# Kernel optimization log

Hardware: AMD Instinct MI355X
Metric: run time of the kernel (lower is better)

Reference implementation:

```python
import jax, jax.numpy as jnp
import numpy as np

DIM = 1024
N_HEADS = 16
HEAD_DIM = 64
SEQ = 2048
BATCH = 2


def setup_inputs() -> dict:
    key = jax.random.key(0)
    ks = jax.random.split(key, 7)
    scale = 1.0 / np.sqrt(DIM)
    return {
        "q": jax.random.normal(ks[0], (BATCH, SEQ, DIM), dtype=jnp.float32),
        "k": jax.random.normal(ks[1], (BATCH, SEQ, DIM), dtype=jnp.float32),
        "v": jax.random.normal(ks[2], (BATCH, SEQ, DIM), dtype=jnp.float32),
        "wq": jax.random.normal(ks[3], (DIM, DIM), dtype=jnp.float32) * scale,
        "wk": jax.random.normal(ks[4], (DIM, DIM), dtype=jnp.float32) * scale,
        "wv": jax.random.normal(ks[5], (DIM, DIM), dtype=jnp.float32) * scale,
        "wo": jax.random.normal(ks[6], (DIM, DIM), dtype=jnp.float32) * scale,
    }


def reference(q, k, v, wq, wk, wv, wo):
    B, S, D = q.shape
    # Linear layers: y = x @ W.T (torch nn.Linear convention)
    qh = (q @ wq.T).reshape(B, S, N_HEADS, HEAD_DIM).transpose(0, 2, 1, 3)  # [B,H,S,hd]
    kh = (k @ wk.T).reshape(B, S, N_HEADS, HEAD_DIM).transpose(0, 2, 1, 3)
    vh = (v @ wv.T).reshape(B, S, N_HEADS, HEAD_DIM).transpose(0, 2, 1, 3)
    score = jnp.einsum('bhqd,bhkd->bhqk', qh, kh) / jnp.sqrt(jnp.float32(HEAD_DIM))
    # causal mask: upper triangle (j > i) set to -inf
    causal = jnp.tril(jnp.ones((S, S), dtype=bool))
    score = jnp.where(causal[None, None], score, -jnp.inf)
    attn = jax.nn.softmax(score, axis=-1)
    out = jnp.einsum('bhqk,bhkd->bhqd', attn, vh)  # [B,H,S,hd]
    out = out.transpose(0, 2, 1, 3).reshape(B, S, D)
    return out @ wo.T
```

## Files before the change

### kernel.cpp

```cpp
#include <hip/hip_runtime.h>

typedef unsigned short u16;
typedef unsigned int   u32;
typedef __bf16 bf16x8 __attribute__((ext_vector_type(8)));
typedef float  f32x4  __attribute__((ext_vector_type(4)));
typedef unsigned short u16x4 __attribute__((ext_vector_type(4)));
typedef unsigned short u16x8 __attribute__((ext_vector_type(8)));
typedef unsigned int   u32x2 __attribute__((ext_vector_type(2)));
typedef unsigned int   u32x4 __attribute__((ext_vector_type(4)));

#define DIM   1024
#define SEQ   2048
#define NH    16
#define HD    64
#define NBATCH 2

#define NEG_INF (-__builtin_inff())
#define QSCALE 0.1803368801111204f


__device__ __forceinline__ u16 f2bf(float f) {
  unsigned u = __float_as_uint(f);
  unsigned r = (u + 0x7FFFu + ((u >> 16) & 1u)) >> 16;
  return (u16)r;
}

__device__ __forceinline__ u32 pkbf(float a, float b) {
#if __has_builtin(__builtin_amdgcn_cvt_pk_bf16_f32)
  typedef __bf16 bf16x2 __attribute__((ext_vector_type(2)));
  bf16x2 t = __builtin_amdgcn_cvt_pk_bf16_f32(a, b);
  return __builtin_bit_cast(u32, t);
#else
  return (u32)f2bf(a) | ((u32)f2bf(b) << 16);
#endif
}

__device__ __forceinline__ void gload16(const void* g, void* lds_uniform) {
  __builtin_amdgcn_global_load_lds(
      (__attribute__((address_space(1))) void*)(size_t)g,
      (__attribute__((address_space(3))) void*)lds_uniform,
      16, 0, 0);
}


__global__ __launch_bounds__(256) void cvt_all(
    const float* __restrict__ q, const float* __restrict__ k, const float* __restrict__ v,
    const float* __restrict__ wq, const float* __restrict__ wk, const float* __restrict__ wv,
    const float* __restrict__ wo, u16* __restrict__ ws) {
  const size_t M = 1u << 20;
  int b = blockIdx.x;
  const float* src;
  u16* dst;
  int idx;
  if (b < 6144) {
    int t = b >> 11; idx = b & 2047;
    src = (t == 0) ? q : (t == 1) ? k : v;
    dst = ws + (size_t)t * 4 * M;
  } else {
    int t = (b - 6144) >> 9; idx = (b - 6144) & 511;
    src = (t == 0) ? wq : (t == 1) ? wk : (t == 2) ? wv : wo;
    dst = ws + (12 + (size_t)t) * M;
  }
  size_t i = ((size_t)idx * 256 + threadIdx.x) * 8;
  float4 a = *(const float4*)(src + i);
  float4 c = *(const float4*)(src + i + 4);
  u16x8 o;
  o[0] = f2bf(a.x); o[1] = f2bf(a.y); o[2] = f2bf(a.z); o[3] = f2bf(a.w);
  o[4] = f2bf(c.x); o[5] = f2bf(c.y); o[6] = f2bf(c.z); o[7] = f2bf(c.w);
  *(u16x8*)(dst + i) = o;
}


__device__ __forceinline__ void gemm128_core(const u16* __restrict__ A,
                                             const u16* __restrict__ W,
                                             int bm, int bn,
                                             u16* lds, f32x4 (&acc)[4][4]) {
  const int K = 1024;
  const int tid = threadIdx.x;
  const int wave = tid >> 6, lane = tid & 63;
  const int quad = lane >> 4, l15 = lane & 15;
  const int warp_m = wave >> 1, warp_n = wave & 1;

  const int c0 = wave * 128 + lane, c1 = c0 + 64;
  const u16* Ag0 = A + (size_t)(bm * 128 + (c0 >> 2)) * K + (c0 & 3) * 8;
  const u16* Ag1 = A + (size_t)(bm * 128 + (c1 >> 2)) * K + (c1 & 3) * 8;
  const u16* Wg0 = W + (size_t)(bn * 128 + (c0 >> 2)) * K + (c0 & 3) * 8;
  const u16* Wg1 = W + (size_t)(bn * 128 + (c1 >> 2)) * K + (c1 & 3) * 8;
  const int lA0 = (wave * 2 + 0) * 512;
  const int lA1 = (wave * 2 + 1) * 512;
  const int lB0 = 4096 + (wave * 2 + 0) * 512;
  const int lB1 = 4096 + (wave * 2 + 1) * 512;

  gload16(Ag0, lds + lA0);
  gload16(Ag1, lds + lA1);
  gload16(Wg0, lds + lB0);
  gload16(Wg1, lds + lB1);

  for (int k0 = 0; k0 < K; k0 += 32) {
    const int buf = (k0 >> 5) & 1;
    u16* cur = lds + buf * 8192;
    __syncthreads();
    if (k0 + 32 < K) {
      u16* nxt = lds + (buf ^ 1) * 8192;
      gload16(Ag0 + k0 + 32, nxt + lA0);
      gload16(Ag1 + k0 + 32, nxt + lA1);
      gload16(Wg0 + k0 + 32, nxt + lB0);
      gload16(Wg1 + k0 + 32, nxt + lB1);
    }

    bf16x8 af[4], bfr[4];
#pragma unroll
    for (int i = 0; i < 4; ++i) {
      af[i]  = *(const bf16x8*)(cur + (warp_m * 64 + i * 16 + l15) * 32 + quad * 8);
      bfr[i] = *(const bf16x8*)(cur + 4096 + (warp_n * 64 + i * 16 + l15) * 32 + quad * 8);
    }
#pragma unroll
    for (int i = 0; i < 4; ++i)
#pragma unroll
      for (int j = 0; j < 4; ++j)
        acc[i][j] = __builtin_amdgcn_mfma_f32_16x16x32_bf16(af[i], bfr[j], acc[i][j], 0, 0, 0);
  }
}

__global__ __launch_bounds__(256) void gemm_qkv(
    const u16* __restrict__ qb, const u16* __restrict__ kb, const u16* __restrict__ vb,
    const u16* __restrict__ wq, const u16* __restrict__ wk, const u16* __restrict__ wv,
    u16* __restrict__ Qo, u16* __restrict__ Ko, u16* __restrict__ Vt) {
  __shared__ __align__(16) u16 lds[2][8192];
  const int id = blockIdx.x;
  const int c = id & 7, bn = (id >> 3) & 7, t = id >> 6;
  const int g = c + 8 * t;
  const int bm = g & 31, z = g >> 5;

  const u16* A = (z == 0) ? qb : (z == 1) ? kb : vb;
  const u16* W = (z == 0) ? wq : (z == 1) ? wk : wv;
  f32x4 acc[4][4] = {};
  gemm128_core(A, W, bm, bn, &lds[0][0], acc);

  const int tid = threadIdx.x;
  const int wave = tid >> 6, lane = tid & 63;
  const int quad = lane >> 4, l15 = lane & 15;
  const int warp_m = wave >> 1, warp_n = wave & 1;
#pragma unroll
  for (int i = 0; i < 4; ++i)
#pragma unroll
    for (int j = 0; j < 4; ++j) {
      int s0 = bm * 128 + warp_m * 64 + i * 16 + quad * 4;
      int n  = bn * 128 + warp_n * 64 + j * 16 + l15;
      int bb = s0 >> 11, sl0 = s0 & 2047, h = n >> 6, d = n & 63;
      if (z == 2) {
        int pos = (sl0 & ~63) | (sl0 & 32) | ((sl0 & 12) << 1) | ((sl0 & 16) >> 2);
        int psw = (pos & ~63) | ((((pos >> 3) & 7) ^ (d & 7)) << 3) | (pos & 7);
        u16x4 pv;
        pv[0] = f2bf(acc[i][j][0]); pv[1] = f2bf(acc[i][j][1]);
        pv[2] = f2bf(acc[i][j][2]); pv[3] = f2bf(acc[i][j][3]);
        *(u16x4*)(Vt + ((size_t)(bb * NH + h) * HD + d) * SEQ + psw) = pv;
      } else if (z == 1) {
#pragma unroll
        for (int r = 0; r < 4; ++r) {
          int s = sl0 + r;
          int dsw = (((d >> 3) ^ (s & 7)) << 3) | (d & 7);
          Ko[((size_t)(bb * NH + h) * SEQ + s) * HD + dsw] = f2bf(acc[i][j][r]);
        }
      } else {
#pragma unroll
        for (int r = 0; r < 4; ++r)
          Qo[((size_t)(bb * NH + h) * SEQ + sl0 + r) * HD + d] = f2bf(acc[i][j][r] * QSCALE);
      }
    }
}

__global__ __launch_bounds__(256) void gemm_out(
    const u16* __restrict__ A, const u16* __restrict__ W, float* __restrict__ Out) {
  __shared__ __align__(16) u16 lds[2][8192];
  const int id = blockIdx.x;
  const int bn = (id >> 3) & 7;
  const int bm = (id & 7) + 8 * (id >> 6);
  f32x4 acc[4][4] = {};
  gemm128_core(A, W, bm, bn, &lds[0][0], acc);

  const int tid = threadIdx.x;
  const int wave = tid >> 6, lane = tid & 63;
  const int quad = lane >> 4, l15 = lane & 15;
  const int warp_m = wave >> 1, warp_n = wave & 1;
#pragma unroll
  for (int i = 0; i < 4; ++i)
#pragma unroll
    for (int j = 0; j < 4; ++j)
#pragma unroll
      for (int r = 0; r < 4; ++r) {
        int m = bm * 128 + warp_m * 64 + i * 16 + quad * 4 + r;
        int n = bn * 128 + warp_n * 64 + j * 16 + l15;
        Out[(size_t)m * DIM + n] = acc[i][j][r];
      }
}


__global__ __launch_bounds__(256) void attn_kernel(
    const u16* __restrict__ Q, const u16* __restrict__ K,
    const u16* __restrict__ Vt, u16* __restrict__ O) {
  __shared__ __align__(16) u16 Kl[2][4096];
  __shared__ __align__(16) u16 Vl[2][4096];

  const int tid = threadIdx.x;
  const int wave = tid >> 6, lane = tid & 63;
  const int quad = lane >> 4, l15 = lane & 15;
  const int bx = blockIdx.x;
  const int bh = bx & 31;
  const int qt = 31 - (bx >> 5);
  const int b = bh >> 4, h = bh & 15;

  const u16* qbase = Q + ((size_t)bh * SEQ + qt * 64 + wave * 16 + l15) * HD + quad * 8;
  const bf16x8 qf0 = *(const bf16x8*)(qbase);
  const bf16x8 qf1 = *(const bf16x8*)(qbase + 32);

  bf16x8 ones;
#pragma unroll
  for (int i = 0; i < 8; ++i) ones[i] = (__bf16)1.0f;

  f32x4 o[4] = {};
  f32x4 o4 = {};
  float m_run = NEG_INF;

  const int c0 = wave * 128 + lane, c1 = c0 + 64;
  const u16* Ksrc = K + (size_t)bh * SEQ * HD;
  const u16* Vsrc = Vt + (size_t)bh * HD * SEQ;
  const int sw0 = ((quad ^ (l15 & 7)) << 3);
  const int sw1 = (((4 + quad) ^ (l15 & 7)) << 3);

  {
    gload16(Ksrc + (size_t)c0 * 8, &Kl[0][(wave * 2 + 0) * 512]);
    gload16(Ksrc + (size_t)c1 * 8, &Kl[0][(wave * 2 + 1) * 512]);
    gload16(Vsrc + (size_t)(c0 >> 3) * SEQ + (c0 & 7) * 8, &Vl[0][(wave * 2 + 0) * 512]);
    gload16(Vsrc + (size_t)(c1 >> 3) * SEQ + (c1 & 7) * 8, &Vl[0][(wave * 2 + 1) * 512]);
  }

  for (int kt = 0; kt <= qt; ++kt) {
    const int buf = kt & 1;
    __syncthreads();
    if (kt < qt) {
      const int nb = buf ^ 1;
      const size_t kb = (size_t)(kt + 1) * 64;
      gload16(Ksrc + (kb * HD) + (size_t)c0 * 8, &Kl[nb][(wave * 2 + 0) * 512]);
      gload16(Ksrc + (kb * HD) + (size_t)c1 * 8, &Kl[nb][(wave * 2 + 1) * 512]);
      gload16(Vsrc + (size_t)(c0 >> 3) * SEQ + kb + (c0 & 7) * 8, &Vl[nb][(wave * 2 + 0) * 512]);
      gload16(Vsrc + (size_t)(c1 >> 3) * SEQ + kb + (c1 & 7) * 8, &Vl[nb][(wave * 2 + 1) * 512]);
    }

    f32x4 s[4];
#pragma unroll
    for (int kn = 0; kn < 4; ++kn) {
      const u16* arow = &Kl[buf][(kn * 16 + l15) * 64];
      bf16x8 kf0 = *(const bf16x8*)(arow + sw0);
      bf16x8 kf1 = *(const bf16x8*)(arow + sw1);
      f32x4 z = {};
      z = __builtin_amdgcn_mfma_f32_16x16x32_bf16(kf0, qf0, z, 0, 0, 0);
      z = __builtin_amdgcn_mfma_f32_16x16x32_bf16(kf1, qf1, z, 0, 0, 0);
      s[kn] = z;
    }

    if (kt == qt) {
      const int qloc = wave * 16 + l15;
#pragma unroll
      for (int kn = 0; kn < 4; ++kn)
#pragma unroll
        for (int r = 0; r < 4; ++r)
          if (kn * 16 + quad * 4 + r > qloc) s[kn][r] = NEG_INF;
    }

    float mr = NEG_INF;
#pragma unroll
    for (int kn = 0; kn < 4; ++kn)
#pragma unroll
      for (int r = 0; r < 4; ++r) mr = fmaxf(mr, s[kn][r]);
    mr = fmaxf(mr, __shfl_xor(mr, 16));
    mr = fmaxf(mr, __shfl_xor(mr, 32));
    const float mnew = fmaxf(m_run, mr);
    const float alpha = __builtin_amdgcn_exp2f(m_run - mnew);
    m_run = mnew;
#pragma unroll
    for (int kn = 0; kn < 4; ++kn)
#pragma unroll
      for (int r = 0; r < 4; ++r)
        s[kn][r] = __builtin_amdgcn_exp2f(s[kn][r] - mnew);

    u32x4 t0, t1;
    t0[0] = pkbf(s[0][0], s[0][1]); t0[1] = pkbf(s[0][2], s[0][3]);
    t0[2] = pkbf(s[1][0], s[1][1]); t0[3] = pkbf(s[1][2], s[1][3]);
    t1[0] = pkbf(s[2][0], s[2][1]); t1[1] = pkbf(s[2][2], s[2][3]);
    t1[2] = pkbf(s[3][0], s[3][1]); t1[3] = pkbf(s[3][2], s[3][3]);
    bf16x8 pf0 = __builtin_bit_cast(bf16x8, t0);
    bf16x8 pf1 = __builtin_bit_cast(bf16x8, t1);

#pragma unroll
    for (int n = 0; n < 4; ++n)
#pragma unroll
      for (int r = 0; r < 4; ++r) o[n][r] *= alpha;
#pragma unroll
    for (int r = 0; r < 4; ++r) o4[r] *= alpha;

    o4 = __builtin_amdgcn_mfma_f32_16x16x32_bf16(ones, pf0, o4, 0, 0, 0);
    o4 = __builtin_amdgcn_mfma_f32_16x16x32_bf16(ones, pf1, o4, 0, 0, 0);

#pragma unroll
    for (int n = 0; n < 4; ++n) {
      const u16* vrow = &Vl[buf][(n * 16 + l15) * 64];
      bf16x8 vf0 = *(const bf16x8*)(vrow + sw0);
      bf16x8 vf1 = *(const bf16x8*)(vrow + sw1);
      o[n] = __builtin_amdgcn_mfma_f32_16x16x32_bf16(vf0, pf0, o[n], 0, 0, 0);
      o[n] = __builtin_amdgcn_mfma_f32_16x16x32_bf16(vf1, pf1, o[n], 0, 0, 0);
    }
  }

  const float inv = 1.f / o4[0];
  const int srow = qt * 64 + wave * 16 + l15;
  u16* obase = O + ((size_t)b * SEQ + srow) * DIM + h * HD + quad * 4;
#pragma unroll
  for (int n = 0; n < 4; ++n) {
    u32x2 st;
    st[0] = pkbf(o[n][0] * inv, o[n][1] * inv);
    st[1] = pkbf(o[n][2] * inv, o[n][3] * inv);
    *(u32x2*)(obase + n * 16) = st;
  }
}


extern "C" void kernel_launch(void* const* d_in, const int* in_sizes, int n_in,
                              void* d_out, int out_size, void* d_ws, size_t ws_size,
                              hipStream_t stream) {
  (void)in_sizes; (void)n_in; (void)out_size; (void)ws_size;
  const float* q  = (const float*)d_in[0];
  const float* k  = (const float*)d_in[1];
  const float* v  = (const float*)d_in[2];
  const float* wq = (const float*)d_in[3];
  const float* wk = (const float*)d_in[4];
  const float* wv = (const float*)d_in[5];
  const float* wo = (const float*)d_in[6];

  u16* ws = (u16*)d_ws;
  const size_t EL = 1u << 20;
  u16* QB = ws + 0 * EL;
  u16* KB = ws + 4 * EL;
  u16* VB = ws + 8 * EL;
  u16* WQ = ws + 12 * EL;
  u16* WK = ws + 13 * EL;
  u16* WV = ws + 14 * EL;
  u16* WO = ws + 15 * EL;
  u16* Qw = ws + 16 * EL;
  u16* Kw = ws + 20 * EL;
  u16* Vtw = ws + 24 * EL;
  u16* AO = ws + 28 * EL;

  cvt_all<<<8192, 256, 0, stream>>>(q, k, v, wq, wk, wv, wo, ws);
  gemm_qkv<<<768, 256, 0, stream>>>(QB, KB, VB, WQ, WK, WV, Qw, Kw, Vtw);
  attn_kernel<<<1024, 256, 0, stream>>>(Qw, Kw, Vtw, AO);
  gemm_out<<<256, 256, 0, stream>>>(AO, WO, (float*)d_out);
}
```

Baseline: 200.6 us.

## Fuse activation bf16 conversion into QKV GEMM, swizzle LDS, retile out-proj

The separate conversion pass over the fp32 q/k/v activations is removed. The QKV GEMM now loads fp32 rows into registers, packs them to bf16 and stores them into LDS with an XOR swizzle, which removes a 48MB-ish round trip through workspace. W and A LDS layouts are swizzled to reduce bank conflicts. The output projection uses 128x64 tiles with 512 blocks for better CU occupancy, and the attention q-tile order is snaked for load balance. The cost is that the QKV GEMM does its A-operand conversion and register staging inside the main loop.

Result: slower. 222.5 us (+10.9%).

```diff
diff --git a/kernel.cpp b/kernel.cpp
--- a/kernel.cpp
+++ b/kernel.cpp
@@ -43,24 +43,15 @@
 }
 
 
-__global__ __launch_bounds__(256) void cvt_all(
-    const float* __restrict__ q, const float* __restrict__ k, const float* __restrict__ v,
-    const float* __restrict__ wq, const float* __restrict__ wk, const float* __restrict__ wv,
-    const float* __restrict__ wo, u16* __restrict__ ws) {
+__global__ __launch_bounds__(256) void cvt_w(
+    const float* __restrict__ wq, const float* __restrict__ wk,
+    const float* __restrict__ wv, const float* __restrict__ wo,
+    u16* __restrict__ ws) {
   const size_t M = 1u << 20;
   int b = blockIdx.x;
-  const float* src;
-  u16* dst;
-  int idx;
-  if (b < 6144) {
-    int t = b >> 11; idx = b & 2047;
-    src = (t == 0) ? q : (t == 1) ? k : v;
-    dst = ws + (size_t)t * 4 * M;
-  } else {
-    int t = (b - 6144) >> 9; idx = (b - 6144) & 511;
-    src = (t == 0) ? wq : (t == 1) ? wk : (t == 2) ? wv : wo;
-    dst = ws + (12 + (size_t)t) * M;
-  }
+  int t = b >> 9, idx = b & 511;
+  const float* src = (t == 0) ? wq : (t == 1) ? wk : (t == 2) ? wv : wo;
+  u16* dst = ws + (size_t)t * M;
   size_t i = ((size_t)idx * 256 + threadIdx.x) * 8;
   float4 a = *(const float4*)(src + i);
   float4 c = *(const float4*)(src + i + 4);
@@ -71,10 +62,10 @@
 }
 
 
-__device__ __forceinline__ void gemm128_core(const u16* __restrict__ A,
-                                             const u16* __restrict__ W,
-                                             int bm, int bn,
-                                             u16* lds, f32x4 (&acc)[4][4]) {
+__device__ __forceinline__ void gemm128f_core(const float* __restrict__ A,
+                                              const u16* __restrict__ W,
+                                              int bm, int bn,
+                                              u16* lds, f32x4 (&acc)[4][4]) {
   const int K = 1024;
   const int tid = threadIdx.x;
   const int wave = tid >> 6, lane = tid & 63;
@@ -82,37 +73,55 @@
   const int warp_m = wave >> 1, warp_n = wave & 1;
 
   const int c0 = wave * 128 + lane, c1 = c0 + 64;
-  const u16* Ag0 = A + (size_t)(bm * 128 + (c0 >> 2)) * K + (c0 & 3) * 8;
-  const u16* Ag1 = A + (size_t)(bm * 128 + (c1 >> 2)) * K + (c1 & 3) * 8;
-  const u16* Wg0 = W + (size_t)(bn * 128 + (c0 >> 2)) * K + (c0 & 3) * 8;
-  const u16* Wg1 = W + (size_t)(bn * 128 + (c1 >> 2)) * K + (c1 & 3) * 8;
-  const int lA0 = (wave * 2 + 0) * 512;
-  const int lA1 = (wave * 2 + 1) * 512;
+  const u16* Wg0 = W + (size_t)(bn * 128 + (c0 >> 2)) * K + (((c0 & 3) ^ ((c0 >> 3) & 3)) * 8);
+  const u16* Wg1 = W + (size_t)(bn * 128 + (c1 >> 2)) * K + (((c1 & 3) ^ ((c1 >> 3) & 3)) * 8);
   const int lB0 = 4096 + (wave * 2 + 0) * 512;
   const int lB1 = 4096 + (wave * 2 + 1) * 512;
 
-  gload16(Ag0, lds + lA0);
-  gload16(Ag1, lds + lA1);
+  const float* Ag[4];
+  int adst[4];
+#pragma unroll
+  for (int j = 0; j < 4; ++j) {
+    int ca = wave * 256 + 64 * j + lane;
+    int row = ca >> 3, ch = ca & 7;
+    Ag[j] = A + (size_t)(bm * 128 + row) * K + ch * 4;
+    adst[j] = row * 32 + (((ch >> 1) ^ ((row >> 1) & 3)) << 3) + (ch & 1) * 4;
+  }
+
+  float4 r[4];
+#pragma unroll
+  for (int j = 0; j < 4; ++j) r[j] = *(const float4*)(Ag[j]);
   gload16(Wg0, lds + lB0);
   gload16(Wg1, lds + lB1);
 
   for (int k0 = 0; k0 < K; k0 += 32) {
     const int buf = (k0 >> 5) & 1;
     u16* cur = lds + buf * 8192;
+
+#pragma unroll
+    for (int j = 0; j < 4; ++j) {
+      u32x2 wv;
+      wv[0] = pkbf(r[j].x, r[j].y);
+      wv[1] = pkbf(r[j].z, r[j].w);
+      *(u32x2*)(cur + adst[j]) = wv;
+    }
     __syncthreads();
+
     if (k0 + 32 < K) {
       u16* nxt = lds + (buf ^ 1) * 8192;
-      gload16(Ag0 + k0 + 32, nxt + lA0);
-      gload16(Ag1 + k0 + 32, nxt + lA1);
       gload16(Wg0 + k0 + 32, nxt + lB0);
       gload16(Wg1 + k0 + 32, nxt + lB1);
+#pragma unroll
+      for (int j = 0; j < 4; ++j) r[j] = *(const float4*)(Ag[j] + k0 + 32);
     }
 
     bf16x8 af[4], bfr[4];
 #pragma unroll
     for (int i = 0; i < 4; ++i) {
-      af[i]  = *(const bf16x8*)(cur + (warp_m * 64 + i * 16 + l15) * 32 + quad * 8);
-      bfr[i] = *(const bf16x8*)(cur + 4096 + (warp_n * 64 + i * 16 + l15) * 32 + quad * 8);
+      int ra = warp_m * 64 + i * 16 + l15;
+      int rb = warp_n * 64 + i * 16 + l15;
+      af[i]  = *(const bf16x8*)(cur + ra * 32 + ((quad ^ ((ra >> 1) & 3)) << 3));
+      bfr[i] = *(const bf16x8*)(cur + 4096 + rb * 32 + ((quad ^ ((rb >> 1) & 3)) << 3));
     }
 #pragma unroll
     for (int i = 0; i < 4; ++i)
@@ -123,7 +132,7 @@
 }
 
 __global__ __launch_bounds__(256) void gemm_qkv(
-    const u16* __restrict__ qb, const u16* __restrict__ kb, const u16* __restrict__ vb,
+    const float* __restrict__ qb, const float* __restrict__ kb, const float* __restrict__ vb,
     const u16* __restrict__ wq, const u16* __restrict__ wk, const u16* __restrict__ wv,
     u16* __restrict__ Qo, u16* __restrict__ Ko, u16* __restrict__ Vt) {
   __shared__ __align__(16) u16 lds[2][8192];
@@ -132,10 +141,10 @@
   const int g = c + 8 * t;
   const int bm = g & 31, z = g >> 5;
 
-  const u16* A = (z == 0) ? qb : (z == 1) ? kb : vb;
+  const float* A = (z == 0) ? qb : (z == 1) ? kb : vb;
   const u16* W = (z == 0) ? wq : (z == 1) ? wk : wv;
   f32x4 acc[4][4] = {};
-  gemm128_core(A, W, bm, bn, &lds[0][0], acc);
+  gemm128f_core(A, W, bm, bn, &lds[0][0], acc);
 
   const int tid = threadIdx.x;
   const int wave = tid >> 6, lane = tid & 63;
@@ -172,25 +181,67 @@
 
 __global__ __launch_bounds__(256) void gemm_out(
     const u16* __restrict__ A, const u16* __restrict__ W, float* __restrict__ Out) {
-  __shared__ __align__(16) u16 lds[2][8192];
+  __shared__ __align__(16) u16 lds[2][6144];
+  const int K = 1024;
   const int id = blockIdx.x;
-  const int bn = (id >> 3) & 7;
-  const int bm = (id & 7) + 8 * (id >> 6);
-  f32x4 acc[4][4] = {};
-  gemm128_core(A, W, bm, bn, &lds[0][0], acc);
-
+  const int bn = (id >> 3) & 15;
+  const int bm = (id & 7) + 8 * (id >> 7);
   const int tid = threadIdx.x;
   const int wave = tid >> 6, lane = tid & 63;
   const int quad = lane >> 4, l15 = lane & 15;
   const int warp_m = wave >> 1, warp_n = wave & 1;
+
+  const int c0 = wave * 128 + lane, c1 = c0 + 64;
+  const u16* Ag0 = A + (size_t)(bm * 128 + (c0 >> 2)) * K + (((c0 & 3) ^ ((c0 >> 3) & 3)) * 8);
+  const u16* Ag1 = A + (size_t)(bm * 128 + (c1 >> 2)) * K + (((c1 & 3) ^ ((c1 >> 3) & 3)) * 8);
+  const int cw = wave * 64 + lane;
+  const u16* Wg = W + (size_t)(bn * 64 + (cw >> 2)) * K + (((cw & 3) ^ ((cw >> 3) & 3)) * 8);
+  const int lA0 = (wave * 2 + 0) * 512;
+  const int lA1 = (wave * 2 + 1) * 512;
+  const int lB  = 4096 + wave * 512;
+
+  u16* lds0 = &lds[0][0];
+  gload16(Ag0, lds0 + lA0);
+  gload16(Ag1, lds0 + lA1);
+  gload16(Wg,  lds0 + lB);
+
+  f32x4 acc[4][2] = {};
+  for (int k0 = 0; k0 < K; k0 += 32) {
+    const int buf = (k0 >> 5) & 1;
+    u16* cur = lds0 + buf * 6144;
+    __syncthreads();
+    if (k0 + 32 < K) {
+      u16* nxt = lds0 + (buf ^ 1) * 6144;
+      gload16(Ag0 + k0 + 32, nxt + lA0);
+      gload16(Ag1 + k0 + 32, nxt + lA1);
+      gload16(Wg  + k0 + 32, nxt + lB);
+    }
+    bf16x8 af[4], bfr[2];
+#pragma unroll
+    for (int i = 0; i < 4; ++i) {
+      int ra = warp_m * 64 + i * 16 + l15;
+      af[i] = *(const bf16x8*)(cur + ra * 32 + ((quad ^ ((ra >> 1) & 3)) << 3));
+    }
+#pragma unroll
+    for (int j = 0; j < 2; ++j) {
+      int rb = warp_n * 32 + j * 16 + l15;
+      bfr[j] = *(const bf16x8*)(cur + 4096 + rb * 32 + ((quad ^ ((rb >> 1) & 3)) << 3));
+    }
+#pragma unroll
+    for (int i = 0; i < 4; ++i)
+#pragma unroll
+      for (int j = 0; j < 2; ++j)
+        acc[i][j] = __builtin_amdgcn_mfma_f32_16x16x32_bf16(af[i], bfr[j], acc[i][j], 0, 0, 0);
+  }
+
 #pragma unroll
   for (int i = 0; i < 4; ++i)
 #pragma unroll
-    for (int j = 0; j < 4; ++j)
+    for (int j = 0; j < 2; ++j)
 #pragma unroll
       for (int r = 0; r < 4; ++r) {
         int m = bm * 128 + warp_m * 64 + i * 16 + quad * 4 + r;
-        int n = bn * 128 + warp_n * 64 + j * 16 + l15;
+        int n = bn * 64 + warp_n * 32 + j * 16 + l15;
         Out[(size_t)m * DIM + n] = acc[i][j][r];
       }
 }
@@ -207,7 +258,8 @@
   const int quad = lane >> 4, l15 = lane & 15;
   const int bx = blockIdx.x;
   const int bh = bx & 31;
-  const int qt = 31 - (bx >> 5);
+  const int j = bx >> 5, jhi = j >> 3, jlo = j & 7;
+  const int qt = 31 - (jhi * 8 + ((jhi & 1) ? (7 - jlo) : jlo));
   const int b = bh >> 4, h = bh & 15;
 
   const u16* qbase = Q + ((size_t)bh * SEQ + qt * 64 + wave * 16 + l15) * HD + quad * 8;
@@ -339,20 +391,17 @@
 
   u16* ws = (u16*)d_ws;
   const size_t EL = 1u << 20;
-  u16* QB = ws + 0 * EL;
-  u16* KB = ws + 4 * EL;
-  u16* VB = ws + 8 * EL;
-  u16* WQ = ws + 12 * EL;
-  u16* WK = ws + 13 * EL;
-  u16* WV = ws + 14 * EL;
-  u16* WO = ws + 15 * EL;
-  u16* Qw = ws + 16 * EL;
-  u16* Kw = ws + 20 * EL;
-  u16* Vtw = ws + 24 * EL;
-  u16* AO = ws + 28 * EL;
-
-  cvt_all<<<8192, 256, 0, stream>>>(q, k, v, wq, wk, wv, wo, ws);
-  gemm_qkv<<<768, 256, 0, stream>>>(QB, KB, VB, WQ, WK, WV, Qw, Kw, Vtw);
+  u16* WQ = ws + 0 * EL;
+  u16* WK = ws + 1 * EL;
+  u16* WV = ws + 2 * EL;
+  u16* WO = ws + 3 * EL;
+  u16* Qw = ws + 4 * EL;
+  u16* Kw = ws + 8 * EL;
+  u16* Vtw = ws + 12 * EL;
+  u16* AO = ws + 16 * EL;
+
+  cvt_w<<<2048, 256, 0, stream>>>(wq, wk, wv, wo, ws);
+  gemm_qkv<<<768, 256, 0, stream>>>(q, k, v, WQ, WK, WV, Qw, Kw, Vtw);
   attn_kernel<<<1024, 256, 0, stream>>>(Qw, Kw, Vtw, AO);
-  gemm_out<<<256, 256, 0, stream>>>(AO, WO, (float*)d_out);
-}
+  gemm_out<<<512, 256, 0, stream>>>(AO, WO, (float*)d_out);
+}
```
